# Performance work log

Measured on AMD Instinct MI355X. Metric: run time of the kernel, lower is better.

## Reference

```python
import jax, jax.numpy as jnp
import numpy as np

B, T, F, H = 4096, 64, 64, 128
EPS = 1e-12


def setup_inputs() -> dict:
    key = jax.random.key(0)
    ks = jax.random.split(key, 16)
    inp = {
        "values": jax.random.normal(ks[0], (B, T, F), jnp.float32),
        "masks": (jax.random.uniform(ks[1], (B, T, F)) < 0.8).astype(jnp.float32),
        "deltas": jax.random.uniform(ks[2], (B, T, F), jnp.float32) * 5.0,
        # TemporalDecay h: Linear(F -> H)
        "W_dh": jax.random.normal(ks[3], (H, F), jnp.float32) / np.sqrt(F),
        "b_dh": jnp.zeros((H,), jnp.float32),
        # TemporalDecay x (diag): Linear(F -> F) with identity mask on W
        "W_dx": jax.random.normal(ks[4], (F, F), jnp.float32) / np.sqrt(F),
        "b_dx": jnp.zeros((F,), jnp.float32),
        # hist_reg: Linear(H -> F)
        "W_hist": jax.random.normal(ks[5], (F, H), jnp.float32) / np.sqrt(H),
        "b_hist": jnp.zeros((F,), jnp.float32),
        # feat_reg: Linear(F -> F) with zeroed diagonal
        "W_feat": jax.random.normal(ks[6], (F, F), jnp.float32) / np.sqrt(F),
        "b_feat": jnp.zeros((F,), jnp.float32),
        # combining_weight: Linear(2F -> F)
        "W_comb": jax.random.normal(ks[7], (F, 2 * F), jnp.float32) / np.sqrt(2 * F),
        "b_comb": jnp.zeros((F,), jnp.float32),
        # LSTMCell(2F -> H): gate order i, f, g, o
        "W_ih": jax.random.normal(ks[8], (4 * H, 2 * F), jnp.float32) / np.sqrt(2 * F),
        "b_ih": jnp.zeros((4 * H,), jnp.float32),
        "W_hh": jax.random.normal(ks[9], (4 * H, H), jnp.float32) / np.sqrt(H),
        "b_hh": jnp.zeros((4 * H,), jnp.float32),
    }
    return inp


def _masked_mae(pred, target, mask):
    return jnp.sum(jnp.abs(pred - target) * mask) / (jnp.sum(mask) + EPS)


def _rits(values, masks, deltas, W_dh, b_dh, W_dx, b_dx, W_hist, b_hist,
          W_feat, b_feat, W_comb, b_comb, W_ih, b_ih, W_hh, b_hh):
    n_steps = values.shape[1]
    eyeF = jnp.eye(values.shape[2], dtype=values.dtype)
    Wdx_diag = W_dx * eyeF            # diag=True temporal decay
    Wfeat_od = W_feat * (1.0 - eyeF)

    def step(carry, xs):
        h, c, loss = carry
        x, m, d = xs  # each [B, F]
        gamma_h = jnp.exp(-jax.nn.relu(d @ W_dh.T + b_dh))    # [B, H]
        gamma_x = jnp.exp(-jax.nn.relu(d @ Wdx_diag.T + b_dx))  # [B, F]
        h = h * gamma_h
        x_h = h @ W_hist.T + b_hist
        loss = loss + _masked_mae(x_h, x, m)
        x_c = m * x + (1.0 - m) * x_h
        z_h = x_c @ Wfeat_od.T + b_feat
        loss = loss + _masked_mae(z_h, x, m)
        alpha = jax.nn.sigmoid(jnp.concatenate([gamma_x, m], axis=1) @ W_comb.T + b_comb)
        c_h = alpha * z_h + (1.0 - alpha) * x_h
        loss = loss + _masked_mae(c_h, x, m)
        c_c = m * x + (1.0 - m) * c_h
        inp = jnp.concatenate([c_c, m], axis=1)  # [B, 2F]
        gates = inp @ W_ih.T + b_ih + h @ W_hh.T + b_hh
        i, f, g, o = jnp.split(gates, 4, axis=-1)
        c = jax.nn.sigmoid(f) * c + jax.nn.sigmoid(i) * jnp.tanh(g)
        h = jax.nn.sigmoid(o) * jnp.tanh(c)
        return (h, c, loss), c_h

    h0 = jnp.zeros((values.shape[0], W_hh.shape[1]), values.dtype)
    c0 = jnp.zeros_like(h0)
    xs = (jnp.swapaxes(values, 0, 1), jnp.swapaxes(masks, 0, 1), jnp.swapaxes(deltas, 0, 1))
    (h, c, loss), est_t = jax.lax.scan(step, (h0, c0, jnp.float32(0.0)), xs)
    estimations = jnp.swapaxes(est_t, 0, 1)  # [B, T, F]
    imputed = masks * values + (1.0 - masks) * estimations
    recon_loss = loss / (n_steps * 3)
    return imputed, estimations, h, recon_loss


def reference(values, masks, deltas, W_dh, b_dh, W_dx, b_dx, W_hist, b_hist,
              W_feat, b_feat, W_comb, b_comb, W_ih, b_ih, W_hh, b_hh):
    return _rits(values, masks, deltas, W_dh, b_dh, W_dx, b_dx, W_hist, b_hist,
                 W_feat, b_feat, W_comb, b_comb, W_ih, b_ih, W_hh, b_hh)
```

## Files before the change

kernel.cpp:

```cpp
#include <hip/hip_runtime.h>

typedef float f32x4 __attribute__((ext_vector_type(4)));
typedef unsigned int u32x2 __attribute__((ext_vector_type(2)));
typedef __bf16 bf16x2 __attribute__((ext_vector_type(2)));
typedef __bf16 bf16x8 __attribute__((ext_vector_type(8)));

static_assert(sizeof(bf16x8) == 16, "bf16x8 must be 16B");

#define NB 4096
#define NT 64
#define NBLK 256
#define BTF (NB * NT * 64)

#define LGKM_BAR() do { \
    asm volatile("s_waitcnt lgkmcnt(0)" ::: "memory"); \
    __builtin_amdgcn_s_barrier(); \
  } while (0)

__device__ __forceinline__ unsigned short f2bf(float x) {
  return __builtin_bit_cast(unsigned short, (__bf16)x);
}
__device__ __forceinline__ unsigned int pk2(float lo, float hi) {
  bf16x2 t; t[0] = (__bf16)lo; t[1] = (__bf16)hi;
  return __builtin_bit_cast(unsigned int, t);
}
__device__ __forceinline__ float bf2f(unsigned int us) {
  return __builtin_bit_cast(float, us << 16);
}

__device__ __forceinline__ f32x4 mfma16(bf16x8 a, bf16x8 b, f32x4 c) {
  return __builtin_amdgcn_mfma_f32_16x16x32_bf16(a, b, c, 0, 0, 0);
}

__device__ __forceinline__ bf16x8 cvt8(f32x4 a, f32x4 b) {
  bf16x8 r;
#pragma unroll
  for (int j = 0; j < 4; ++j) { r[j] = (__bf16)a[j]; r[4 + j] = (__bf16)b[j]; }
  return r;
}

__device__ __forceinline__ bf16x8 loadW8(const float* __restrict__ row, int k0) {
  f32x4 a = *(const f32x4*)(row + k0);
  f32x4 b = *(const f32x4*)(row + k0 + 4);
  return cvt8(a, b);
}

__device__ __forceinline__ bf16x8 loadW8zd(const float* __restrict__ row, int k0, int col) {
  f32x4 a = *(const f32x4*)(row + k0);
  f32x4 b = *(const f32x4*)(row + k0 + 4);
  bf16x8 r;
#pragma unroll
  for (int j = 0; j < 4; ++j) {
    r[j]     = (k0 + j     == col) ? (__bf16)0.f : (__bf16)a[j];
    r[4 + j] = (k0 + 4 + j == col) ? (__bf16)0.f : (__bf16)b[j];
  }
  return r;
}

__device__ __forceinline__ float sigm(float x) { return 1.f / (1.f + __expf(-x)); }
__device__ __forceinline__ float tanh_fast(float x) { return 1.f - 2.f / (__expf(2.f * x) + 1.f); }

__global__ __launch_bounds__(512, 2) void rits_main_kernel(
    const float* __restrict__ values, const float* __restrict__ masks,
    const float* __restrict__ deltas,
    const float* __restrict__ W_dh, const float* __restrict__ b_dh,
    const float* __restrict__ W_dx, const float* __restrict__ b_dx,
    const float* __restrict__ W_hist, const float* __restrict__ b_hist,
    const float* __restrict__ W_feat, const float* __restrict__ b_feat,
    const float* __restrict__ W_comb, const float* __restrict__ b_comb,
    const float* __restrict__ W_ih, const float* __restrict__ b_ih,
    const float* __restrict__ W_hh, const float* __restrict__ b_hh,
    float* __restrict__ out_imp, float* __restrict__ out_est,
    float* __restrict__ out_h, float* __restrict__ loss_ws) {
  const int tid = threadIdx.x;
  const int w = tid >> 6;
  const int l = tid & 63;
  const int rA = l & 15;
  const int kg = l >> 4;
  const int wg = blockIdx.x;
  const int b0 = wg * 16;
  const int colh = w * 16 + rA;
  const int colw = (w & 3) * 16 + rA;
  const int s = tid & 255;
  const int sr = s >> 4, sq = s & 15;

  __shared__ float sX[2][16][68];
  __shared__ unsigned short sMb[2][16][72], sDb[2][16][72];
  __shared__ unsigned short sHb[2][16][136];
  __shared__ unsigned short sXcb[16][72], sCcb[16][72];
  __shared__ unsigned short sGxb[16][72];
  __shared__ float sAlT[64][20];
  __shared__ float sCh[16][68], sCc[16][68];
  __shared__ float sWdxB[128];
  __shared__ float sLoss[4][4];

  if (tid < 64)       sWdxB[tid] = W_dx[tid * 65];
  else if (tid < 128) sWdxB[tid] = b_dx[tid - 64];
#pragma unroll
  for (int i = 0; i < 4; ++i) sHb[0][kg * 4 + i][colh] = 0;

  bf16x8 wgf[4][8];
#pragma unroll
  for (int g = 0; g < 4; ++g) {
    int col = g * 128 + colh;
#pragma unroll
    for (int kk = 0; kk < 4; ++kk) wgf[g][kk] = loadW8(W_ih + (size_t)col * 128, kk * 32 + kg * 8);
#pragma unroll
    for (int kk = 0; kk < 4; ++kk) wgf[g][4 + kk] = loadW8(W_hh + (size_t)col * 128, kk * 32 + kg * 8);
  }
  bf16x8 wdhf[2];
#pragma unroll
  for (int kk = 0; kk < 2; ++kk) wdhf[kk] = loadW8(W_dh + (size_t)colh * 64, kk * 32 + kg * 8);

  bf16x8 wsm[4], wfeat[2];
  if (w < 4) {
#pragma unroll
    for (int kk = 0; kk < 4; ++kk) wsm[kk] = loadW8(W_hist + (size_t)colw * 128, kk * 32 + kg * 8);
#pragma unroll
    for (int kk = 0; kk < 2; ++kk) wfeat[kk] = loadW8zd(W_feat + (size_t)colw * 64, kk * 32 + kg * 8, colw);
  } else {
#pragma unroll
    for (int kk = 0; kk < 4; ++kk) wsm[kk] = loadW8(W_comb + (size_t)colw * 128, kk * 32 + kg * 8);
#pragma unroll
    for (int kk = 0; kk < 2; ++kk) { bf16x8 z = {}; wfeat[kk] = z; }
  }

  const float bdh = b_dh[colh];
  const float bhist = (w < 4) ? b_hist[colw] : 0.f;
  const float bfeat = (w < 4) ? b_feat[colw] : 0.f;
  const float bcomb = (w >= 4) ? b_comb[colw] : 0.f;
  float bg[4];
#pragma unroll
  for (int g = 0; g < 4; ++g) bg[g] = b_ih[g * 128 + colh] + b_hh[g * 128 + colh];

  f32x4 h_reg = {0.f, 0.f, 0.f, 0.f};
  f32x4 c_reg = {0.f, 0.f, 0.f, 0.f};

  const size_t gbase = (size_t)(b0 + sr) * 4096 + sq * 4;
  const int orow = (tid & 255) >> 4, oq = tid & 15;
  float* pout = ((tid < 256) ? out_est : out_imp) + (size_t)(b0 + orow) * 4096 + oq * 4;
  const float* sOut0 = (tid < 256) ? &sCh[orow][oq * 4] : &sCc[orow][oq * 4];

  if (w >= 4) {
    f32x4 vx0 = *(const f32x4*)&values[gbase];
    f32x4 vm0 = *(const f32x4*)&masks[gbase];
    f32x4 vd0 = *(const f32x4*)&deltas[gbase];
    *(f32x4*)&sX[0][sr][sq * 4] = vx0;
    u32x2 pm, pd;
    pm[0] = pk2(vm0[0], vm0[1]); pm[1] = pk2(vm0[2], vm0[3]);
    pd[0] = pk2(vd0[0], vd0[1]); pd[1] = pk2(vd0[2], vd0[3]);
    *(u32x2*)&sMb[0][sr][sq * 4] = pm;
    *(u32x2*)&sDb[0][sr][sq * 4] = pd;
  }
  LGKM_BAR();

  f32x4 vx, vm, vd;
  if (w >= 4) {
    vx = *(const f32x4*)&values[gbase + 64];
    vm = *(const f32x4*)&masks[gbase + 64];
    vd = *(const f32x4*)&deltas[gbase + 64];
  }
  {
    int e = tid * 2, rr = e >> 6, f0 = e & 63;
    unsigned int dp = *(const unsigned int*)&sDb[0][rr][f0];
    float g0 = __expf(-fmaxf(bf2f(dp & 0xffffu) * sWdxB[f0]     + sWdxB[64 + f0],     0.f));
    float g1 = __expf(-fmaxf(bf2f(dp >> 16)     * sWdxB[f0 + 1] + sWdxB[64 + f0 + 1], 0.f));
    *(unsigned int*)&sGxb[rr][f0] = pk2(g0, g1);
  }
  LGKM_BAR();

  for (int t = 0; t < NT; ++t) {
    const int p = t & 1;

    if (t > 0 && tid < 4) {
      float ls = sLoss[0][tid] + sLoss[1][tid] + sLoss[2][tid] + sLoss[3][tid];
      loss_ws[((size_t)(t - 1) * NBLK + wg) * 4 + tid] = ls;
    }
    float xh[4], xr[4], mr[4];
    float n1 = 0.f, n2 = 0.f, n3 = 0.f, den = 0.f;
    if (w < 4) {
      f32x4 axh = {0.f, 0.f, 0.f, 0.f};
#pragma unroll
      for (int kk = 0; kk < 4; ++kk) {
        bf16x8 a = *(const bf16x8*)&sHb[p][rA][kk * 32 + kg * 8];
        axh = mfma16(a, wsm[kk], axh);
      }
#pragma unroll
      for (int i = 0; i < 4; ++i) {
        int row = kg * 4 + i;
        xr[i] = sX[p][row][colw];
        mr[i] = bf2f(sMb[p][row][colw]);
        xh[i] = axh[i] + bhist;
        float xc = mr[i] * xr[i] + (1.f - mr[i]) * xh[i];
        sXcb[row][colw] = f2bf(xc);
      }
    } else {
      f32x4 aal = {0.f, 0.f, 0.f, 0.f};
      bf16x8 a0 = *(const bf16x8*)&sGxb[rA][kg * 8];
      bf16x8 a1 = *(const bf16x8*)&sGxb[rA][32 + kg * 8];
      aal = mfma16(a0, wsm[0], aal);
      aal = mfma16(a1, wsm[1], aal);
      bf16x8 a2 = *(const bf16x8*)&sMb[p][rA][kg * 8];
      bf16x8 a3 = *(const bf16x8*)&sMb[p][rA][32 + kg * 8];
      aal = mfma16(a2, wsm[2], aal);
      aal = mfma16(a3, wsm[3], aal);
      f32x4 alv;
#pragma unroll
      for (int i = 0; i < 4; ++i) alv[i] = sigm(aal[i] + bcomb);
      *(f32x4*)&sAlT[colw][kg * 4] = alv;
#pragma unroll
      for (int i = 0; i < 4; ++i) { xh[i] = 0.f; xr[i] = 0.f; mr[i] = 0.f; }
    }
    LGKM_BAR();

    f32x4 acc[4];
#pragma unroll
    for (int g = 0; g < 4; ++g) { f32x4 z = {0.f, 0.f, 0.f, 0.f}; acc[g] = z; }
    if (w < 4) {
      f32x4 azh = {0.f, 0.f, 0.f, 0.f};
      bf16x8 ax0 = *(const bf16x8*)&sXcb[rA][kg * 8];
      bf16x8 ax1 = *(const bf16x8*)&sXcb[rA][32 + kg * 8];
      azh = mfma16(ax0, wfeat[0], azh);
      azh = mfma16(ax1, wfeat[1], azh);
      f32x4 alv = *(const f32x4*)&sAlT[colw][kg * 4];
#pragma unroll
      for (int i = 0; i < 4; ++i) {
        int row = kg * 4 + i;
        float zh = azh[i] + bfeat;
        float al = alv[i];
        float ch = al * zh + (1.f - al) * xh[i];
        float cc = mr[i] * xr[i] + (1.f - mr[i]) * ch;
        sCh[row][colw] = ch;
        sCc[row][colw] = cc;
        sCcb[row][colw] = f2bf(cc);
        n1 += fabsf(xh[i] - xr[i]) * mr[i];
        n2 += fabsf(zh - xr[i]) * mr[i];
        n3 += fabsf(ch - xr[i]) * mr[i];
        den += mr[i];
      }
    } else {
      *(f32x4*)&sX[p ^ 1][sr][sq * 4] = vx;
      u32x2 pm, pd;
      pm[0] = pk2(vm[0], vm[1]); pm[1] = pk2(vm[2], vm[3]);
      pd[0] = pk2(vd[0], vd[1]); pd[1] = pk2(vd[2], vd[3]);
      *(u32x2*)&sMb[p ^ 1][sr][sq * 4] = pm;
      *(u32x2*)&sDb[p ^ 1][sr][sq * 4] = pd;
    }
    {
      bf16x8 fm0 = *(const bf16x8*)&sMb[p][rA][kg * 8];
      bf16x8 fm1 = *(const bf16x8*)&sMb[p][rA][32 + kg * 8];
      bf16x8 fh0 = *(const bf16x8*)&sHb[p][rA][kg * 8];
      bf16x8 fh1 = *(const bf16x8*)&sHb[p][rA][32 + kg * 8];
      bf16x8 fh2 = *(const bf16x8*)&sHb[p][rA][64 + kg * 8];
      bf16x8 fh3 = *(const bf16x8*)&sHb[p][rA][96 + kg * 8];
#pragma unroll
      for (int g = 0; g < 4; ++g) acc[g] = mfma16(fm0, wgf[g][2], acc[g]);
#pragma unroll
      for (int g = 0; g < 4; ++g) acc[g] = mfma16(fm1, wgf[g][3], acc[g]);
#pragma unroll
      for (int g = 0; g < 4; ++g) acc[g] = mfma16(fh0, wgf[g][4], acc[g]);
#pragma unroll
      for (int g = 0; g < 4; ++g) acc[g] = mfma16(fh1, wgf[g][5], acc[g]);
#pragma unroll
      for (int g = 0; g < 4; ++g) acc[g] = mfma16(fh2, wgf[g][6], acc[g]);
#pragma unroll
      for (int g = 0; g < 4; ++g) acc[g] = mfma16(fh3, wgf[g][7], acc[g]);
    }
    LGKM_BAR();

    if (w >= 4) {
      int tq = (t + 2 <= NT - 1) ? t + 2 : NT - 1;
      size_t ga = gbase + (size_t)(tq << 6);
      vx = *(const f32x4*)&values[ga];
      vm = *(const f32x4*)&masks[ga];
      vd = *(const f32x4*)&deltas[ga];
    }
    *(f32x4*)pout = *(const f32x4*)sOut0;
    pout += 64;
    {
      bf16x8 ac0 = *(const bf16x8*)&sCcb[rA][kg * 8];
      bf16x8 ac1 = *(const bf16x8*)&sCcb[rA][32 + kg * 8];
#pragma unroll
      for (int g = 0; g < 4; ++g) acc[g] = mfma16(ac0, wgf[g][0], acc[g]);
#pragma unroll
      for (int g = 0; g < 4; ++g) acc[g] = mfma16(ac1, wgf[g][1], acc[g]);
    }
    if (w < 4) {
#pragma unroll
      for (int off = 32; off > 0; off >>= 1) {
        n1 += __shfl_down(n1, off);
        n2 += __shfl_down(n2, off);
        n3 += __shfl_down(n3, off);
        den += __shfl_down(den, off);
      }
      if (l == 0) {
        f32x4 lv; lv[0] = n1; lv[1] = n2; lv[2] = n3; lv[3] = den;
        *(f32x4*)&sLoss[w][0] = lv;
      }
    }
#pragma unroll
    for (int i = 0; i < 4; ++i) {
      float ii = sigm(acc[0][i] + bg[0]);
      float ff = sigm(acc[1][i] + bg[1]);
      float g_ = tanh_fast(acc[2][i] + bg[2]);
      float oo = sigm(acc[3][i] + bg[3]);
      float c_ = ff * c_reg[i] + ii * g_;
      c_reg[i] = c_;
      h_reg[i] = oo * tanh_fast(c_);
    }
    if (t < NT - 1) {
      bf16x8 a0 = *(const bf16x8*)&sDb[p ^ 1][rA][kg * 8];
      bf16x8 a1 = *(const bf16x8*)&sDb[p ^ 1][rA][32 + kg * 8];
      f32x4 ga4 = {0.f, 0.f, 0.f, 0.f};
      ga4 = mfma16(a0, wdhf[0], ga4);
      ga4 = mfma16(a1, wdhf[1], ga4);
#pragma unroll
      for (int i = 0; i < 4; ++i) {
        float g = __expf(-fmaxf(ga4[i] + bdh, 0.f));
        h_reg[i] *= g;
        sHb[p ^ 1][kg * 4 + i][colh] = f2bf(h_reg[i]);
      }
      int e = tid * 2, rr = e >> 6, f0 = e & 63;
      unsigned int dp = *(const unsigned int*)&sDb[p ^ 1][rr][f0];
      float g0 = __expf(-fmaxf(bf2f(dp & 0xffffu) * sWdxB[f0]     + sWdxB[64 + f0],     0.f));
      float g1 = __expf(-fmaxf(bf2f(dp >> 16)     * sWdxB[f0 + 1] + sWdxB[64 + f0 + 1], 0.f));
      *(unsigned int*)&sGxb[rr][f0] = pk2(g0, g1);
    } else {
#pragma unroll
      for (int i = 0; i < 4; ++i) out_h[(size_t)(b0 + kg * 4 + i) * 128 + colh] = h_reg[i];
    }
    LGKM_BAR();
  }

  if (tid < 4) {
    float ls = sLoss[0][tid] + sLoss[1][tid] + sLoss[2][tid] + sLoss[3][tid];
    loss_ws[((size_t)(NT - 1) * NBLK + wg) * 4 + tid] = ls;
  }
}

__global__ void rits_loss_kernel(const float* __restrict__ ws, float* __restrict__ out_loss) {
  int tid = threadIdx.x;
  float n1 = 0.f, n2 = 0.f, n3 = 0.f, den = 0.f;
  for (int g = 0; g < NBLK; ++g) {
    const float* p = &ws[((size_t)tid * NBLK + g) * 4];
    n1 += p[0]; n2 += p[1]; n3 += p[2]; den += p[3];
  }
  float lt = (n1 + n2 + n3) / (den + 1e-12f);
#pragma unroll
  for (int off = 32; off > 0; off >>= 1) lt += __shfl_down(lt, off);
  if (tid == 0) out_loss[0] = lt / 192.f;
}

extern "C" void kernel_launch(void* const* d_in, const int* in_sizes, int n_in,
                              void* d_out, int out_size, void* d_ws, size_t ws_size,
                              hipStream_t stream) {
  const float* values = (const float*)d_in[0];
  const float* masks  = (const float*)d_in[1];
  const float* deltas = (const float*)d_in[2];
  const float* W_dh   = (const float*)d_in[3];
  const float* b_dh   = (const float*)d_in[4];
  const float* W_dx   = (const float*)d_in[5];
  const float* b_dx   = (const float*)d_in[6];
  const float* W_hist = (const float*)d_in[7];
  const float* b_hist = (const float*)d_in[8];
  const float* W_feat = (const float*)d_in[9];
  const float* b_feat = (const float*)d_in[10];
  const float* W_comb = (const float*)d_in[11];
  const float* b_comb = (const float*)d_in[12];
  const float* W_ih   = (const float*)d_in[13];
  const float* b_ih   = (const float*)d_in[14];
  const float* W_hh   = (const float*)d_in[15];
  const float* b_hh   = (const float*)d_in[16];

  float* out = (float*)d_out;
  float* out_imp = out;
  float* out_est = out + (size_t)BTF;
  float* out_h   = out + (size_t)2 * BTF;
  float* out_ls  = out + (size_t)2 * BTF + (size_t)NB * 128;
  float* loss_ws = (float*)d_ws;

  rits_main_kernel<<<NBLK, 512, 0, stream>>>(
      values, masks, deltas, W_dh, b_dh, W_dx, b_dx, W_hist, b_hist,
      W_feat, b_feat, W_comb, b_comb, W_ih, b_ih, W_hh, b_hh,
      out_imp, out_est, out_h, loss_ws);
  rits_loss_kernel<<<1, 64, 0, stream>>>(loss_ws, out_ls);
}
```

Baseline: 257.3 us.

## Split RITS step across 16 waves with dedicated h@W_hh and I/O waves

Doubles the block to 1024 threads and gives work to specialised waves. Eight waves compute the h@W_hh gate partials and pass them through shared memory, while the other eight handle the input-side gates, regression and LSTM update. The small regression weights move from registers to shared memory, and loss reduction, prefetch and output stores go to dedicated waves. The aim is a shorter per-step critical path, at the cost of an extra shared-memory round trip for gate partials, more LDS use and one block per CU.

```diff
diff --git a/kernel.cpp b/kernel.cpp
--- a/kernel.cpp
+++ b/kernel.cpp
@@ -2,6 +2,7 @@
 
 typedef float f32x4 __attribute__((ext_vector_type(4)));
 typedef unsigned int u32x2 __attribute__((ext_vector_type(2)));
+typedef unsigned short u16x4 __attribute__((ext_vector_type(4)));
 typedef __bf16 bf16x2 __attribute__((ext_vector_type(2)));
 typedef __bf16 bf16x8 __attribute__((ext_vector_type(8)));
 
@@ -60,7 +61,9 @@
 __device__ __forceinline__ float sigm(float x) { return 1.f / (1.f + __expf(-x)); }
 __device__ __forceinline__ float tanh_fast(float x) { return 1.f - 2.f / (__expf(2.f * x) + 1.f); }
 
-__global__ __launch_bounds__(512, 2) void rits_main_kernel(
+__device__ __forceinline__ f32x4 splat4(float v) { f32x4 r; r[0]=v; r[1]=v; r[2]=v; r[3]=v; return r; }
+
+__global__ __launch_bounds__(1024, 1) void rits_main_kernel(
     const float* __restrict__ values, const float* __restrict__ masks,
     const float* __restrict__ deltas,
     const float* __restrict__ W_dh, const float* __restrict__ b_dh,
@@ -79,213 +82,246 @@
   const int kg = l >> 4;
   const int wg = blockIdx.x;
   const int b0 = wg * 16;
-  const int colh = w * 16 + rA;
-  const int colw = (w & 3) * 16 + rA;
-  const int s = tid & 255;
-  const int sr = s >> 4, sq = s & 15;
+  const int colF = (w & 3) * 16 + rA;
+  const int colH = (w & 7) * 16 + rA;
 
   __shared__ float sX[2][16][68];
   __shared__ unsigned short sMb[2][16][72], sDb[2][16][72];
   __shared__ unsigned short sHb[2][16][136];
-  __shared__ unsigned short sXcb[16][72], sCcb[16][72];
+  __shared__ unsigned short sXcb[16][72], sCcb[16][72], sXhb[16][72], sZhb[16][72];
   __shared__ unsigned short sGxb[16][72];
-  __shared__ float sAlT[64][20];
   __shared__ float sCh[16][68], sCc[16][68];
+  __shared__ float sGPT[512][20];
+  __shared__ unsigned short sWh[64][136];
+  __shared__ unsigned short sWc[64][136];
+  __shared__ unsigned short sWf[64][72];
   __shared__ float sWdxB[128];
   __shared__ float sLoss[4][4];
 
+  {
+    int c = tid >> 4, k0 = (tid & 15) * 8;
+    *(bf16x8*)&sWh[c][k0] = loadW8(W_hist + (size_t)c * 128, k0);
+    *(bf16x8*)&sWc[c][k0] = loadW8(W_comb + (size_t)c * 128, k0);
+  }
+  if (tid < 512) {
+    int c = tid >> 3, k0 = (tid & 7) * 8;
+    *(bf16x8*)&sWf[c][k0] = loadW8zd(W_feat + (size_t)c * 64, k0, c);
+  }
   if (tid < 64)       sWdxB[tid] = W_dx[tid * 65];
   else if (tid < 128) sWdxB[tid] = b_dx[tid - 64];
-#pragma unroll
-  for (int i = 0; i < 4; ++i) sHb[0][kg * 4 + i][colh] = 0;
-
-  bf16x8 wgf[4][8];
-#pragma unroll
-  for (int g = 0; g < 4; ++g) {
-    int col = g * 128 + colh;
-#pragma unroll
-    for (int kk = 0; kk < 4; ++kk) wgf[g][kk] = loadW8(W_ih + (size_t)col * 128, kk * 32 + kg * 8);
-#pragma unroll
-    for (int kk = 0; kk < 4; ++kk) wgf[g][4 + kk] = loadW8(W_hh + (size_t)col * 128, kk * 32 + kg * 8);
+  if (w < 8) {
+#pragma unroll
+    for (int i = 0; i < 4; ++i) sHb[0][kg * 4 + i][colH] = 0;
+  }
+
+  bf16x8 wgf[4][4];
+  if (w < 8) {
+#pragma unroll
+    for (int g = 0; g < 4; ++g) {
+      int col = g * 128 + colH;
+#pragma unroll
+      for (int kk = 0; kk < 4; ++kk) wgf[g][kk] = loadW8(W_ih + (size_t)col * 128, kk * 32 + kg * 8);
+    }
+  } else {
+#pragma unroll
+    for (int g = 0; g < 4; ++g) {
+      int col = g * 128 + colH;
+#pragma unroll
+      for (int kk = 0; kk < 4; ++kk) wgf[g][kk] = loadW8(W_hh + (size_t)col * 128, kk * 32 + kg * 8);
+    }
   }
   bf16x8 wdhf[2];
-#pragma unroll
-  for (int kk = 0; kk < 2; ++kk) wdhf[kk] = loadW8(W_dh + (size_t)colh * 64, kk * 32 + kg * 8);
-
-  bf16x8 wsm[4], wfeat[2];
-  if (w < 4) {
-#pragma unroll
-    for (int kk = 0; kk < 4; ++kk) wsm[kk] = loadW8(W_hist + (size_t)colw * 128, kk * 32 + kg * 8);
-#pragma unroll
-    for (int kk = 0; kk < 2; ++kk) wfeat[kk] = loadW8zd(W_feat + (size_t)colw * 64, kk * 32 + kg * 8, colw);
+  if (w < 8) {
+#pragma unroll
+    for (int kk = 0; kk < 2; ++kk) wdhf[kk] = loadW8(W_dh + (size_t)colH * 64, kk * 32 + kg * 8);
   } else {
-#pragma unroll
-    for (int kk = 0; kk < 4; ++kk) wsm[kk] = loadW8(W_comb + (size_t)colw * 128, kk * 32 + kg * 8);
-#pragma unroll
-    for (int kk = 0; kk < 2; ++kk) { bf16x8 z = {}; wfeat[kk] = z; }
-  }
-
-  const float bdh = b_dh[colh];
-  const float bhist = (w < 4) ? b_hist[colw] : 0.f;
-  const float bfeat = (w < 4) ? b_feat[colw] : 0.f;
-  const float bcomb = (w >= 4) ? b_comb[colw] : 0.f;
-  float bg[4];
-#pragma unroll
-  for (int g = 0; g < 4; ++g) bg[g] = b_ih[g * 128 + colh] + b_hh[g * 128 + colh];
+    bf16x8 z = {}; wdhf[0] = z; wdhf[1] = z;
+  }
+
+  float bg[4] = {0.f, 0.f, 0.f, 0.f};
+  float bdh = 0.f, bhist = 0.f, bcomb = 0.f, bfeat = 0.f;
+  if (w < 8) {
+#pragma unroll
+    for (int g = 0; g < 4; ++g) bg[g] = b_ih[g * 128 + colH] + b_hh[g * 128 + colH];
+    bdh = b_dh[colH];
+    if (w < 4) bhist = b_hist[colF];
+    else       { bcomb = b_comb[colF]; bfeat = b_feat[colF]; }
+  }
 
   f32x4 h_reg = {0.f, 0.f, 0.f, 0.f};
   f32x4 c_reg = {0.f, 0.f, 0.f, 0.f};
 
-  const size_t gbase = (size_t)(b0 + sr) * 4096 + sq * 4;
-  const int orow = (tid & 255) >> 4, oq = tid & 15;
-  float* pout = ((tid < 256) ? out_est : out_imp) + (size_t)(b0 + orow) * 4096 + oq * 4;
-  const float* sOut0 = (tid < 256) ? &sCh[orow][oq * 4] : &sCc[orow][oq * 4];
-
-  if (w >= 4) {
+  const int sidx = tid - 512;
+  const int ssr = (sidx & 255) >> 4, ssq = sidx & 15;
+  const size_t gbase = (size_t)(b0 + ssr) * 4096 + ssq * 4;
+  const int oidx = tid - 768;
+  const int orow = (oidx & 255) >> 4, oq = oidx & 15;
+  float* pE = out_est + (size_t)(b0 + orow) * 4096 + oq * 4;
+  float* pI = out_imp + (size_t)(b0 + orow) * 4096 + oq * 4;
+
+  f32x4 vx, vm, vd;
+  if (w >= 8 && w < 12) {
     f32x4 vx0 = *(const f32x4*)&values[gbase];
     f32x4 vm0 = *(const f32x4*)&masks[gbase];
     f32x4 vd0 = *(const f32x4*)&deltas[gbase];
-    *(f32x4*)&sX[0][sr][sq * 4] = vx0;
+    *(f32x4*)&sX[0][ssr][ssq * 4] = vx0;
     u32x2 pm, pd;
     pm[0] = pk2(vm0[0], vm0[1]); pm[1] = pk2(vm0[2], vm0[3]);
     pd[0] = pk2(vd0[0], vd0[1]); pd[1] = pk2(vd0[2], vd0[3]);
-    *(u32x2*)&sMb[0][sr][sq * 4] = pm;
-    *(u32x2*)&sDb[0][sr][sq * 4] = pd;
+    *(u32x2*)&sMb[0][ssr][ssq * 4] = pm;
+    *(u32x2*)&sDb[0][ssr][ssq * 4] = pd;
   }
   LGKM_BAR();
-
-  f32x4 vx, vm, vd;
-  if (w >= 4) {
+  if (tid < 256) {
+    int row = tid >> 4, f0 = (tid & 15) * 4;
+    u32x2 dp = *(const u32x2*)&sDb[0][row][f0];
+    float g0 = __expf(-fmaxf(bf2f(dp[0] & 0xffffu) * sWdxB[f0]     + sWdxB[64 + f0],     0.f));
+    float g1 = __expf(-fmaxf(bf2f(dp[0] >> 16)     * sWdxB[f0 + 1] + sWdxB[64 + f0 + 1], 0.f));
+    float g2 = __expf(-fmaxf(bf2f(dp[1] & 0xffffu) * sWdxB[f0 + 2] + sWdxB[64 + f0 + 2], 0.f));
+    float g3 = __expf(-fmaxf(bf2f(dp[1] >> 16)     * sWdxB[f0 + 3] + sWdxB[64 + f0 + 3], 0.f));
+    u32x2 gp; gp[0] = pk2(g0, g1); gp[1] = pk2(g2, g3);
+    *(u32x2*)&sGxb[row][f0] = gp;
+  }
+  if (w >= 8 && w < 12) {
     vx = *(const f32x4*)&values[gbase + 64];
     vm = *(const f32x4*)&masks[gbase + 64];
     vd = *(const f32x4*)&deltas[gbase + 64];
   }
-  {
-    int e = tid * 2, rr = e >> 6, f0 = e & 63;
-    unsigned int dp = *(const unsigned int*)&sDb[0][rr][f0];
-    float g0 = __expf(-fmaxf(bf2f(dp & 0xffffu) * sWdxB[f0]     + sWdxB[64 + f0],     0.f));
-    float g1 = __expf(-fmaxf(bf2f(dp >> 16)     * sWdxB[f0 + 1] + sWdxB[64 + f0 + 1], 0.f));
-    *(unsigned int*)&sGxb[rr][f0] = pk2(g0, g1);
-  }
   LGKM_BAR();
 
   for (int t = 0; t < NT; ++t) {
     const int p = t & 1;
+    f32x4 acc[4];
+    f32x4 alpha_r = {0.f, 0.f, 0.f, 0.f};
 
     if (t > 0 && tid < 4) {
-      float ls = sLoss[0][tid] + sLoss[1][tid] + sLoss[2][tid] + sLoss[3][tid];
-      loss_ws[((size_t)(t - 1) * NBLK + wg) * 4 + tid] = ls;
-    }
-    float xh[4], xr[4], mr[4];
-    float n1 = 0.f, n2 = 0.f, n3 = 0.f, den = 0.f;
-    if (w < 4) {
-      f32x4 axh = {0.f, 0.f, 0.f, 0.f};
-#pragma unroll
-      for (int kk = 0; kk < 4; ++kk) {
-        bf16x8 a = *(const bf16x8*)&sHb[p][rA][kk * 32 + kg * 8];
-        axh = mfma16(a, wsm[kk], axh);
-      }
+      float lsv = sLoss[0][tid] + sLoss[1][tid] + sLoss[2][tid] + sLoss[3][tid];
+      loss_ws[((size_t)(t - 1) * NBLK + wg) * 4 + tid] = lsv;
+    }
+    if (w < 8) {
+#pragma unroll
+      for (int g = 0; g < 4; ++g) acc[g] = splat4(bg[g]);
+      bf16x8 am0 = *(const bf16x8*)&sMb[p][rA][kg * 8];
+      bf16x8 am1 = *(const bf16x8*)&sMb[p][rA][32 + kg * 8];
+#pragma unroll
+      for (int g = 0; g < 4; ++g) acc[g] = mfma16(am0, wgf[g][2], acc[g]);
+#pragma unroll
+      for (int g = 0; g < 4; ++g) acc[g] = mfma16(am1, wgf[g][3], acc[g]);
+      if (w < 4) {
+        f32x4 axh = splat4(bhist);
+#pragma unroll
+        for (int kk = 0; kk < 4; ++kk) {
+          bf16x8 a = *(const bf16x8*)&sHb[p][rA][kk * 32 + kg * 8];
+          bf16x8 b = *(const bf16x8*)&sWh[colF][kk * 32 + kg * 8];
+          axh = mfma16(a, b, axh);
+        }
+#pragma unroll
+        for (int i = 0; i < 4; ++i) {
+          int row = kg * 4 + i;
+          float xh = axh[i];
+          float xr = sX[p][row][colF];
+          float mr = bf2f(sMb[p][row][colF]);
+          float xc = mr * xr + (1.f - mr) * xh;
+          sXcb[row][colF] = f2bf(xc);
+          sXhb[row][colF] = f2bf(xh);
+        }
+      } else {
+        f32x4 aal = splat4(bcomb);
+        bf16x8 gx0 = *(const bf16x8*)&sGxb[rA][kg * 8];
+        bf16x8 gx1 = *(const bf16x8*)&sGxb[rA][32 + kg * 8];
+        aal = mfma16(gx0, *(const bf16x8*)&sWc[colF][kg * 8], aal);
+        aal = mfma16(gx1, *(const bf16x8*)&sWc[colF][32 + kg * 8], aal);
+        aal = mfma16(am0, *(const bf16x8*)&sWc[colF][64 + kg * 8], aal);
+        aal = mfma16(am1, *(const bf16x8*)&sWc[colF][96 + kg * 8], aal);
+#pragma unroll
+        for (int i = 0; i < 4; ++i) alpha_r[i] = sigm(aal[i]);
+      }
+    } else {
+      f32x4 at[4];
+#pragma unroll
+      for (int g = 0; g < 4; ++g) { f32x4 z = {0.f, 0.f, 0.f, 0.f}; at[g] = z; }
+      bf16x8 ah[4];
+#pragma unroll
+      for (int kk = 0; kk < 4; ++kk) ah[kk] = *(const bf16x8*)&sHb[p][rA][kk * 32 + kg * 8];
+#pragma unroll
+      for (int kk = 0; kk < 4; ++kk)
+#pragma unroll
+        for (int g = 0; g < 4; ++g) at[g] = mfma16(ah[kk], wgf[g][kk], at[g]);
+#pragma unroll
+      for (int g = 0; g < 4; ++g) *(f32x4*)&sGPT[g * 128 + colH][kg * 4] = at[g];
+      if (w < 12) {
+        *(f32x4*)&sX[p ^ 1][ssr][ssq * 4] = vx;
+        u32x2 pm, pd;
+        pm[0] = pk2(vm[0], vm[1]); pm[1] = pk2(vm[2], vm[3]);
+        pd[0] = pk2(vd[0], vd[1]); pd[1] = pk2(vd[2], vd[3]);
+        *(u32x2*)&sMb[p ^ 1][ssr][ssq * 4] = pm;
+        *(u32x2*)&sDb[p ^ 1][ssr][ssq * 4] = pd;
+      }
+    }
+    LGKM_BAR();
+
+    if (w < 8) {
+#pragma unroll
+      for (int g = 0; g < 4; ++g) acc[g] += *(const f32x4*)&sGPT[g * 128 + colH][kg * 4];
+    }
+    if (w >= 4 && w < 8) {
+      f32x4 az = splat4(bfeat);
+      bf16x8 ax0 = *(const bf16x8*)&sXcb[rA][kg * 8];
+      bf16x8 ax1 = *(const bf16x8*)&sXcb[rA][32 + kg * 8];
+      az = mfma16(ax0, *(const bf16x8*)&sWf[colF][kg * 8], az);
+      az = mfma16(ax1, *(const bf16x8*)&sWf[colF][32 + kg * 8], az);
 #pragma unroll
       for (int i = 0; i < 4; ++i) {
         int row = kg * 4 + i;
-        xr[i] = sX[p][row][colw];
-        mr[i] = bf2f(sMb[p][row][colw]);
-        xh[i] = axh[i] + bhist;
-        float xc = mr[i] * xr[i] + (1.f - mr[i]) * xh[i];
-        sXcb[row][colw] = f2bf(xc);
-      }
-    } else {
-      f32x4 aal = {0.f, 0.f, 0.f, 0.f};
-      bf16x8 a0 = *(const bf16x8*)&sGxb[rA][kg * 8];
-      bf16x8 a1 = *(const bf16x8*)&sGxb[rA][32 + kg * 8];
-      aal = mfma16(a0, wsm[0], aal);
-      aal = mfma16(a1, wsm[1], aal);
-      bf16x8 a2 = *(const bf16x8*)&sMb[p][rA][kg * 8];
-      bf16x8 a3 = *(const bf16x8*)&sMb[p][rA][32 + kg * 8];
-      aal = mfma16(a2, wsm[2], aal);
-      aal = mfma16(a3, wsm[3], aal);
-      f32x4 alv;
-#pragma unroll
-      for (int i = 0; i < 4; ++i) alv[i] = sigm(aal[i] + bcomb);
-      *(f32x4*)&sAlT[colw][kg * 4] = alv;
-#pragma unroll
-      for (int i = 0; i < 4; ++i) { xh[i] = 0.f; xr[i] = 0.f; mr[i] = 0.f; }
+        float zh = az[i];
+        float xh = bf2f(sXhb[row][colF]);
+        float al = alpha_r[i];
+        float ch = al * zh + (1.f - al) * xh;
+        float xr = sX[p][row][colF];
+        float mr = bf2f(sMb[p][row][colF]);
+        float cc = mr * xr + (1.f - mr) * ch;
+        sCh[row][colF] = ch;
+        sCc[row][colF] = cc;
+        sCcb[row][colF] = f2bf(cc);
+        sZhb[row][colF] = f2bf(zh);
+      }
+    } else if (w < 4) {
+      int row = tid >> 4, f0 = (tid & 15) * 4;
+      u32x2 dp = *(const u32x2*)&sDb[p ^ 1][row][f0];
+      float g0 = __expf(-fmaxf(bf2f(dp[0] & 0xffffu) * sWdxB[f0]     + sWdxB[64 + f0],     0.f));
+      float g1 = __expf(-fmaxf(bf2f(dp[0] >> 16)     * sWdxB[f0 + 1] + sWdxB[64 + f0 + 1], 0.f));
+      float g2 = __expf(-fmaxf(bf2f(dp[1] & 0xffffu) * sWdxB[f0 + 2] + sWdxB[64 + f0 + 2], 0.f));
+      float g3 = __expf(-fmaxf(bf2f(dp[1] >> 16)     * sWdxB[f0 + 3] + sWdxB[64 + f0 + 3], 0.f));
+      u32x2 gp; gp[0] = pk2(g0, g1); gp[1] = pk2(g2, g3);
+      *(u32x2*)&sGxb[row][f0] = gp;
     }
     LGKM_BAR();
 
-    f32x4 acc[4];
-#pragma unroll
-    for (int g = 0; g < 4; ++g) { f32x4 z = {0.f, 0.f, 0.f, 0.f}; acc[g] = z; }
-    if (w < 4) {
-      f32x4 azh = {0.f, 0.f, 0.f, 0.f};
-      bf16x8 ax0 = *(const bf16x8*)&sXcb[rA][kg * 8];
-      bf16x8 ax1 = *(const bf16x8*)&sXcb[rA][32 + kg * 8];
-      azh = mfma16(ax0, wfeat[0], azh);
-      azh = mfma16(ax1, wfeat[1], azh);
-      f32x4 alv = *(const f32x4*)&sAlT[colw][kg * 4];
-#pragma unroll
-      for (int i = 0; i < 4; ++i) {
-        int row = kg * 4 + i;
-        float zh = azh[i] + bfeat;
-        float al = alv[i];
-        float ch = al * zh + (1.f - al) * xh[i];
-        float cc = mr[i] * xr[i] + (1.f - mr[i]) * ch;
-        sCh[row][colw] = ch;
-        sCc[row][colw] = cc;
-        sCcb[row][colw] = f2bf(cc);
-        n1 += fabsf(xh[i] - xr[i]) * mr[i];
-        n2 += fabsf(zh - xr[i]) * mr[i];
-        n3 += fabsf(ch - xr[i]) * mr[i];
-        den += mr[i];
-      }
-    } else {
-      *(f32x4*)&sX[p ^ 1][sr][sq * 4] = vx;
-      u32x2 pm, pd;
-      pm[0] = pk2(vm[0], vm[1]); pm[1] = pk2(vm[2], vm[3]);
-      pd[0] = pk2(vd[0], vd[1]); pd[1] = pk2(vd[2], vd[3]);
-      *(u32x2*)&sMb[p ^ 1][sr][sq * 4] = pm;
-      *(u32x2*)&sDb[p ^ 1][sr][sq * 4] = pd;
-    }
-    {
-      bf16x8 fm0 = *(const bf16x8*)&sMb[p][rA][kg * 8];
-      bf16x8 fm1 = *(const bf16x8*)&sMb[p][rA][32 + kg * 8];
-      bf16x8 fh0 = *(const bf16x8*)&sHb[p][rA][kg * 8];
-      bf16x8 fh1 = *(const bf16x8*)&sHb[p][rA][32 + kg * 8];
-      bf16x8 fh2 = *(const bf16x8*)&sHb[p][rA][64 + kg * 8];
-      bf16x8 fh3 = *(const bf16x8*)&sHb[p][rA][96 + kg * 8];
-#pragma unroll
-      for (int g = 0; g < 4; ++g) acc[g] = mfma16(fm0, wgf[g][2], acc[g]);
-#pragma unroll
-      for (int g = 0; g < 4; ++g) acc[g] = mfma16(fm1, wgf[g][3], acc[g]);
-#pragma unroll
-      for (int g = 0; g < 4; ++g) acc[g] = mfma16(fh0, wgf[g][4], acc[g]);
-#pragma unroll
-      for (int g = 0; g < 4; ++g) acc[g] = mfma16(fh1, wgf[g][5], acc[g]);
-#pragma unroll
-      for (int g = 0; g < 4; ++g) acc[g] = mfma16(fh2, wgf[g][6], acc[g]);
-#pragma unroll
-      for (int g = 0; g < 4; ++g) acc[g] = mfma16(fh3, wgf[g][7], acc[g]);
-    }
-    LGKM_BAR();
-
-    if (w >= 4) {
+    if (w >= 12) {
+      *(f32x4*)pE = *(const f32x4*)&sCh[orow][oq * 4];
+      *(f32x4*)pI = *(const f32x4*)&sCc[orow][oq * 4];
+      pE += 64; pI += 64;
+    } else if (w >= 8) {
       int tq = (t + 2 <= NT - 1) ? t + 2 : NT - 1;
       size_t ga = gbase + (size_t)(tq << 6);
       vx = *(const f32x4*)&values[ga];
       vm = *(const f32x4*)&masks[ga];
       vd = *(const f32x4*)&deltas[ga];
-    }
-    *(f32x4*)pout = *(const f32x4*)sOut0;
-    pout += 64;
-    {
-      bf16x8 ac0 = *(const bf16x8*)&sCcb[rA][kg * 8];
-      bf16x8 ac1 = *(const bf16x8*)&sCcb[rA][32 + kg * 8];
-#pragma unroll
-      for (int g = 0; g < 4; ++g) acc[g] = mfma16(ac0, wgf[g][0], acc[g]);
-#pragma unroll
-      for (int g = 0; g < 4; ++g) acc[g] = mfma16(ac1, wgf[g][1], acc[g]);
-    }
-    if (w < 4) {
+      f32x4 xv = *(const f32x4*)&sX[p][ssr][ssq * 4];
+      f32x4 chv = *(const f32x4*)&sCh[ssr][ssq * 4];
+      u16x4 mv = *(const u16x4*)&sMb[p][ssr][ssq * 4];
+      u16x4 xhv = *(const u16x4*)&sXhb[ssr][ssq * 4];
+      u16x4 zhv = *(const u16x4*)&sZhb[ssr][ssq * 4];
+      float n1 = 0.f, n2 = 0.f, n3 = 0.f, den = 0.f;
+#pragma unroll
+      for (int j = 0; j < 4; ++j) {
+        float m = bf2f(mv[j]);
+        float x = xv[j];
+        n1 += fabsf(bf2f(xhv[j]) - x) * m;
+        n2 += fabsf(bf2f(zhv[j]) - x) * m;
+        n3 += fabsf(chv[j] - x) * m;
+        den += m;
+      }
 #pragma unroll
       for (int off = 32; off > 0; off >>= 1) {
         n1 += __shfl_down(n1, off);
@@ -295,46 +331,49 @@
       }
       if (l == 0) {
         f32x4 lv; lv[0] = n1; lv[1] = n2; lv[2] = n3; lv[3] = den;
-        *(f32x4*)&sLoss[w][0] = lv;
-      }
-    }
-#pragma unroll
-    for (int i = 0; i < 4; ++i) {
-      float ii = sigm(acc[0][i] + bg[0]);
-      float ff = sigm(acc[1][i] + bg[1]);
-      float g_ = tanh_fast(acc[2][i] + bg[2]);
-      float oo = sigm(acc[3][i] + bg[3]);
-      float c_ = ff * c_reg[i] + ii * g_;
-      c_reg[i] = c_;
-      h_reg[i] = oo * tanh_fast(c_);
-    }
-    if (t < NT - 1) {
-      bf16x8 a0 = *(const bf16x8*)&sDb[p ^ 1][rA][kg * 8];
-      bf16x8 a1 = *(const bf16x8*)&sDb[p ^ 1][rA][32 + kg * 8];
-      f32x4 ga4 = {0.f, 0.f, 0.f, 0.f};
-      ga4 = mfma16(a0, wdhf[0], ga4);
-      ga4 = mfma16(a1, wdhf[1], ga4);
+        *(f32x4*)&sLoss[w - 8][0] = lv;
+      }
+    }
+    if (w < 8) {
+      bf16x8 ac0 = *(const bf16x8*)&sCcb[rA][kg * 8];
+      bf16x8 ac1 = *(const bf16x8*)&sCcb[rA][32 + kg * 8];
+#pragma unroll
+      for (int g = 0; g < 4; ++g) acc[g] = mfma16(ac0, wgf[g][0], acc[g]);
+#pragma unroll
+      for (int g = 0; g < 4; ++g) acc[g] = mfma16(ac1, wgf[g][1], acc[g]);
 #pragma unroll
       for (int i = 0; i < 4; ++i) {
-        float g = __expf(-fmaxf(ga4[i] + bdh, 0.f));
-        h_reg[i] *= g;
-        sHb[p ^ 1][kg * 4 + i][colh] = f2bf(h_reg[i]);
-      }
-      int e = tid * 2, rr = e >> 6, f0 = e & 63;
-      unsigned int dp = *(const unsigned int*)&sDb[p ^ 1][rr][f0];
-      float g0 = __expf(-fmaxf(bf2f(dp & 0xffffu) * sWdxB[f0]     + sWdxB[64 + f0],     0.f));
-      float g1 = __expf(-fmaxf(bf2f(dp >> 16)     * sWdxB[f0 + 1] + sWdxB[64 + f0 + 1], 0.f));
-      *(unsigned int*)&sGxb[rr][f0] = pk2(g0, g1);
-    } else {
-#pragma unroll
-      for (int i = 0; i < 4; ++i) out_h[(size_t)(b0 + kg * 4 + i) * 128 + colh] = h_reg[i];
+        float ii = sigm(acc[0][i]);
+        float ff = sigm(acc[1][i]);
+        float g_ = tanh_fast(acc[2][i]);
+        float oo = sigm(acc[3][i]);
+        float c_ = ff * c_reg[i] + ii * g_;
+        c_reg[i] = c_;
+        h_reg[i] = oo * tanh_fast(c_);
+      }
+      if (t < NT - 1) {
+        f32x4 ga4 = splat4(bdh);
+        bf16x8 a0 = *(const bf16x8*)&sDb[p ^ 1][rA][kg * 8];
+        bf16x8 a1 = *(const bf16x8*)&sDb[p ^ 1][rA][32 + kg * 8];
+        ga4 = mfma16(a0, wdhf[0], ga4);
+        ga4 = mfma16(a1, wdhf[1], ga4);
+#pragma unroll
+        for (int i = 0; i < 4; ++i) {
+          float g = __expf(-fmaxf(ga4[i], 0.f));
+          h_reg[i] *= g;
+          sHb[p ^ 1][kg * 4 + i][colH] = f2bf(h_reg[i]);
+        }
+      } else {
+#pragma unroll
+        for (int i = 0; i < 4; ++i) out_h[(size_t)(b0 + kg * 4 + i) * 128 + colH] = h_reg[i];
+      }
     }
     LGKM_BAR();
   }
 
   if (tid < 4) {
-    float ls = sLoss[0][tid] + sLoss[1][tid] + sLoss[2][tid] + sLoss[3][tid];
-    loss_ws[((size_t)(NT - 1) * NBLK + wg) * 4 + tid] = ls;
+    float lsv = sLoss[0][tid] + sLoss[1][tid] + sLoss[2][tid] + sLoss[3][tid];
+    loss_ws[((size_t)(NT - 1) * NBLK + wg) * 4 + tid] = lsv;
   }
 }
 
@@ -379,7 +418,7 @@
   float* out_ls  = out + (size_t)2 * BTF + (size_t)NB * 128;
   float* loss_ws = (float*)d_ws;
 
-  rits_main_kernel<<<NBLK, 512, 0, stream>>>(
+  rits_main_kernel<<<NBLK, 1024, 0, stream>>>(
       values, masks, deltas, W_dh, b_dh, W_dx, b_dx, W_hist, b_hist,
       W_feat, b_feat, W_comb, b_comb, W_ih, b_ih, W_hh, b_hh,
       out_imp, out_est, out_h, loss_ws);
```

Result: slower. 634.1 us (+146.5%).
